# Kernel optimization log

Hardware: AMD Instinct MI355X
Metric: run time of the kernel (lower is better)

## Reference

```python
import jax, jax.numpy as jnp
import numpy as np

N_NODES = 50000
N_EDGES = 800000
D_IN = 64
F1 = 64
F2 = 64
D_HID = 100


def setup_inputs() -> dict:
    key = jax.random.key(0)
    ks = jax.random.split(key, 12)
    x = jax.random.normal(ks[0], (N_NODES, D_IN), dtype=jnp.float32)
    edge_src = jax.random.randint(ks[1], (N_EDGES,), 0, N_NODES, dtype=jnp.int32)
    edge_dst = jax.random.randint(ks[2], (N_EDGES,), 0, N_NODES, dtype=jnp.int32)
    # stands in for pre-normalized GCN adjacency values (D^-1/2 (A+I) D^-1/2)
    edge_weight = jax.random.uniform(ks[3], (N_EDGES,), dtype=jnp.float32)
    def glorot(k, shape):
        lim = np.sqrt(6.0 / (shape[0] + shape[1]))
        return jax.random.uniform(k, shape, jnp.float32, -lim, lim)
    W1 = glorot(ks[4], (D_IN, F1))
    b1 = jnp.zeros((F1,), jnp.float32)
    W2 = glorot(ks[5], (F1, F2))
    b2 = jnp.zeros((F2,), jnp.float32)
    Wd = glorot(ks[6], (F2, D_HID))
    bd = jnp.zeros((D_HID,), jnp.float32)
    Wo = glorot(ks[7], (D_HID, 1))
    bo = jnp.zeros((1,), jnp.float32)
    return {"x": x, "edge_src": edge_src, "edge_dst": edge_dst,
            "edge_weight": edge_weight, "W1": W1, "b1": b1, "W2": W2,
            "b2": b2, "Wd": Wd, "bd": bd, "Wo": Wo, "bo": bo}


def _gcn_conv(x, edge_src, edge_dst, edge_weight, W, b):
    # spektral GCNConv: out = swish(A_norm @ (X @ W) + b)
    h = x @ W                                        # [N, F]
    msg = h[edge_src] * edge_weight[:, None]          # [E, F] gather + scale
    agg = jax.ops.segment_sum(msg, edge_dst, num_segments=N_NODES)  # [N, F]
    return jax.nn.swish(agg + b)


def reference(x, edge_src, edge_dst, edge_weight, W1, b1, W2, b2, Wd, bd, Wo, bo):
    h = _gcn_conv(x, edge_src, edge_dst, edge_weight, W1, b1)
    h = _gcn_conv(h, edge_src, edge_dst, edge_weight, W2, b2)
    h = jax.nn.swish(h @ Wd + bd)                    # Dense(100, swish)
    return jax.nn.sigmoid(h @ Wo + bo)               # Dense(1, sigmoid) -> [N, 1]
```

## Files before the change

kernel.cpp:

```cpp
#include <hip/hip_runtime.h>
#include <hip/hip_fp16.h>

#define N_NODES 50000
#define N_EDGES 800000
#define D 64
#define DHID 100
#define NTILES (N_NODES / 16)
#define NCT 7
#define CAP 64
#define NGROUPS 4
#define NSLICES 780
#define FILL_BLOCKS (NGROUPS * NSLICES)
#define MM_BLOCKS ((NTILES + 3) / 4)
#define DST_PER_GROUP (N_NODES / NGROUPS)

typedef unsigned short ushort;
typedef unsigned int uint;
typedef __attribute__((ext_vector_type(8))) short s16x8;
typedef __attribute__((ext_vector_type(4))) float f32x4;

#define MFMA16(A, B, C) __builtin_amdgcn_mfma_f32_16x16x32_bf16((A), (B), (C), 0, 0, 0)

__device__ __forceinline__ float swishf(float x) { return x / (1.0f + __expf(-x)); }

__device__ __forceinline__ ushort f2bf(float f) {
    uint u = __float_as_uint(f);
    uint r = (u + 0x7fffu + ((u >> 16) & 1u)) >> 16;
    return (ushort)r;
}
__device__ __forceinline__ float bf2f(ushort h) { return __uint_as_float((uint)h << 16); }
__device__ __forceinline__ float bf_lo(uint d) { return __uint_as_float(d << 16); }
__device__ __forceinline__ float bf_hi(uint d) { return __uint_as_float(d & 0xffff0000u); }

__device__ __forceinline__ float hwf(uint e) {
    return __half2float(__ushort_as_half((ushort)(e >> 16)));
}

__device__ __forceinline__ void accum8(float* acc, uint4 v, float w) {
    acc[0] = fmaf(w, bf_lo(v.x), acc[0]);
    acc[1] = fmaf(w, bf_hi(v.x), acc[1]);
    acc[2] = fmaf(w, bf_lo(v.y), acc[2]);
    acc[3] = fmaf(w, bf_hi(v.y), acc[3]);
    acc[4] = fmaf(w, bf_lo(v.z), acc[4]);
    acc[5] = fmaf(w, bf_hi(v.z), acc[5]);
    acc[6] = fmaf(w, bf_lo(v.w), acc[6]);
    acc[7] = fmaf(w, bf_hi(v.w), acc[7]);
}

__device__ __forceinline__ void gather_node2(const ushort* __restrict__ H,
                                             const uint* __restrict__ bucket,
                                             int degv, int j, int fg, float* acc) {
#pragma unroll
    for (int t = 0; t < 8; ++t) acc[t] = 0.f;
    for (int base = 0; base < degv; base += 16) {
        int s0 = base + j * 4;
        if (s0 < degv) {
            uint4 e = *((const uint4*)(bucket + s0));
            float w0 = hwf(e.x);
            float w1 = (s0 + 1 < degv) ? hwf(e.y) : 0.f;
            float w2 = (s0 + 2 < degv) ? hwf(e.z) : 0.f;
            float w3 = (s0 + 3 < degv) ? hwf(e.w) : 0.f;
            uint s0i = min(e.x & 0xffffu, (uint)(N_NODES - 1));
            uint s1i = min(e.y & 0xffffu, (uint)(N_NODES - 1));
            uint s2i = min(e.z & 0xffffu, (uint)(N_NODES - 1));
            uint s3i = min(e.w & 0xffffu, (uint)(N_NODES - 1));
            uint4 v0 = *((const uint4*)(H + ((size_t)s0i << 6) + (fg << 3)));
            uint4 v1 = *((const uint4*)(H + ((size_t)s1i << 6) + (fg << 3)));
            uint4 v2 = *((const uint4*)(H + ((size_t)s2i << 6) + (fg << 3)));
            uint4 v3 = *((const uint4*)(H + ((size_t)s3i << 6) + (fg << 3)));
            accum8(acc, v0, w0);
            accum8(acc, v1, w1);
            accum8(acc, v2, w2);
            accum8(acc, v3, w3);
        }
    }
#pragma unroll
    for (int t = 0; t < 8; ++t) {
        acc[t] += __shfl_xor(acc[t], 8, 64);
        acc[t] += __shfl_xor(acc[t], 16, 64);
    }
}

__global__ __launch_bounds__(256) void fill_and_l1(const int* __restrict__ src,
                                                   const int* __restrict__ dst,
                                                   const float* __restrict__ w,
                                                   int* __restrict__ deg,
                                                   uint* __restrict__ csr,
                                                   const float* __restrict__ X,
                                                   const float* __restrict__ W,
                                                   const float* __restrict__ W2,
                                                   const float* __restrict__ Wd,
                                                   short* __restrict__ W2T2,
                                                   short* __restrict__ WdT2,
                                                   ushort* __restrict__ H) {
    __shared__ __align__(16) short sBT[2][D][72];
    int tid = threadIdx.x;

    if (blockIdx.x < FILL_BLOCKS) {
        const int g = blockIdx.x & (NGROUPS - 1);
        const int s = blockIdx.x >> 2;
        const int lo = g * DST_PER_GROUP;
        const int hi = lo + DST_PER_GROUP;
        for (int e = s * 256 + tid; e < N_EDGES; e += NSLICES * 256) {
            int d = __builtin_nontemporal_load(dst + e);
            if (d >= lo && d < hi) {
                float wval = __builtin_nontemporal_load(w + e);
                int sval = __builtin_nontemporal_load(src + e);
                uint hw = (uint)__half_as_ushort(__float2half_rn(wval));
                uint payload = (uint)sval | (hw << 16);
                int r = atomicAdd(&deg[d], 1);
                r = min(r, CAP - 1);
                csr[(d << 6) + r] = payload;
            }
        }
        return;
    }

    if (blockIdx.x >= FILL_BLOCKS + MM_BLOCKS) {
        if (blockIdx.x == FILL_BLOCKS + MM_BLOCKS) {
            for (int idx = tid; idx < D * D; idx += 256) {
                int k = idx >> 6, c = idx & 63;
                float wv = W2[idx];
                ushort hi = f2bf(wv);
                W2T2[(size_t)c * D + k] = (short)hi;
                W2T2[(size_t)(D + c) * D + k] = (short)f2bf(wv - bf2f(hi));
            }
        } else {
            for (int idx = tid; idx < NCT * 16 * D; idx += 256) {
                int jj = idx >> 6, k = idx & 63;
                float wv = (jj < DHID) ? Wd[k * DHID + jj] : 0.f;
                ushort hi = f2bf(wv);
                WdT2[(size_t)jj * D + k] = (short)hi;
                WdT2[(size_t)(NCT * 16 + jj) * D + k] = (short)f2bf(wv - bf2f(hi));
            }
        }
        return;
    }

    for (int idx = tid; idx < D * D; idx += 256) {
        int k = idx >> 6, c = idx & 63;
        float wv = W[idx];
        ushort hi = f2bf(wv);
        sBT[0][c][k] = (short)hi;
        sBT[1][c][k] = (short)f2bf(wv - bf2f(hi));
    }
    __syncthreads();
    int wv_ = tid >> 6, lane = tid & 63, quad = lane >> 4, m = lane & 15;
    int tile = min((blockIdx.x - FILL_BLOCKS) * 4 + wv_, NTILES - 1);
    int node0 = tile * 16;

    f32x4 acc[4] = {{0,0,0,0},{0,0,0,0},{0,0,0,0},{0,0,0,0}};
#pragma unroll
    for (int kt = 0; kt < 2; ++kt) {
        int k0 = kt * 32 + quad * 8;
        const float* xp = X + ((size_t)(node0 + m) << 6) + k0;
        f32x4 xa = __builtin_nontemporal_load((const f32x4*)xp);
        f32x4 xb = __builtin_nontemporal_load((const f32x4*)(xp + 4));
        float xv[8] = {xa[0], xa[1], xa[2], xa[3], xb[0], xb[1], xb[2], xb[3]};
        s16x8 ahi, alo;
#pragma unroll
        for (int jj = 0; jj < 8; ++jj) {
            ushort hi = f2bf(xv[jj]);
            ahi[jj] = (short)hi;
            alo[jj] = (short)f2bf(xv[jj] - bf2f(hi));
        }
#pragma unroll
        for (int ct = 0; ct < 4; ++ct) {
            int n = ct * 16 + m;
            s16x8 bhi = *((const s16x8*)&sBT[0][n][k0]);
            s16x8 blo = *((const s16x8*)&sBT[1][n][k0]);
            acc[ct] = MFMA16(ahi, bhi, acc[ct]);
            acc[ct] = MFMA16(ahi, blo, acc[ct]);
            acc[ct] = MFMA16(alo, bhi, acc[ct]);
        }
    }
    __syncthreads();
    short (*rep)[16][72] = (short(*)[16][72])&sBT[0][0][0];
#pragma unroll
    for (int ct = 0; ct < 4; ++ct)
#pragma unroll
        for (int r = 0; r < 4; ++r)
            rep[wv_][quad * 4 + r][ct * 16 + m] = (short)f2bf(acc[ct][r]);
#pragma unroll
    for (int half = 0; half < 2; ++half) {
        int r = (lane >> 3) + half * 8;
        int c0 = (lane & 7) * 8;
        s16x8 v = *((const s16x8*)&rep[wv_][r][c0]);
        *((s16x8*)(H + ((size_t)(node0 + r) << 6) + c0)) = v;
    }
}

__global__ __launch_bounds__(256) void gather_act(const ushort* __restrict__ H,
                                                  const int* __restrict__ deg,
                                                  const uint* __restrict__ csr,
                                                  const float* __restrict__ bias,
                                                  ushort* __restrict__ actOut) {
    int tid = threadIdx.x;
    int wave = tid >> 6, lane = tid & 63;
    int h = lane >> 5, j = (lane >> 3) & 3, fg = lane & 7;
    int node = blockIdx.x * 8 + wave * 2 + h;
    int degv = min(deg[node], CAP);
    const uint* bucket = csr + ((size_t)node << 6);

    float acc[8];
    gather_node2(H, bucket, degv, j, fg, acc);
    if (j == 0) {
        float4 ba = ((const float4*)bias)[fg * 2];
        float4 bb = ((const float4*)bias)[fg * 2 + 1];
        float r0 = swishf(acc[0] + ba.x);
        float r1 = swishf(acc[1] + ba.y);
        float r2 = swishf(acc[2] + ba.z);
        float r3 = swishf(acc[3] + ba.w);
        float r4 = swishf(acc[4] + bb.x);
        float r5 = swishf(acc[5] + bb.y);
        float r6 = swishf(acc[6] + bb.z);
        float r7 = swishf(acc[7] + bb.w);
        uint4 u;
        u.x = (uint)f2bf(r0) | ((uint)f2bf(r1) << 16);
        u.y = (uint)f2bf(r2) | ((uint)f2bf(r3) << 16);
        u.z = (uint)f2bf(r4) | ((uint)f2bf(r5) << 16);
        u.w = (uint)f2bf(r6) | ((uint)f2bf(r7) << 16);
        *((uint4*)(actOut + ((size_t)node << 6) + (fg << 3))) = u;
    }
}

__global__ __launch_bounds__(256) void gather_tail(const ushort* __restrict__ act1,
                                                   const int* __restrict__ deg,
                                                   const uint* __restrict__ csr,
                                                   const short* __restrict__ W2T2,
                                                   const float* __restrict__ b2,
                                                   const short* __restrict__ WdT2,
                                                   const float* __restrict__ bd,
                                                   const float* __restrict__ Wo,
                                                   const float* __restrict__ bo,
                                                   float* __restrict__ out) {
    __shared__ __align__(16) float sAgg[16][72];
    __shared__ __align__(16) short sAct2[16][72];
    __shared__ float sPart[4][16];
    int tid = threadIdx.x;
    int wv = tid >> 6, lane = tid & 63;
    int h = lane >> 5, j = (lane >> 3) & 3, fg = lane & 7;
    int quad = lane >> 4, m = lane & 15;
    int node0 = blockIdx.x * 16;

    for (int t = 0; t < 2; ++t) {
        int nl = wv * 4 + t * 2 + h;
        int node = node0 + nl;
        int degv = min(deg[node], CAP);
        const uint* bucket = csr + ((size_t)node << 6);
        float acc[8];
        gather_node2(act1, bucket, degv, j, fg, acc);
        if (j == 0) {
            float4 u0 = {acc[0], acc[1], acc[2], acc[3]};
            float4 u1 = {acc[4], acc[5], acc[6], acc[7]};
            *((float4*)&sAgg[nl][fg * 8]) = u0;
            *((float4*)&sAgg[nl][fg * 8 + 4]) = u1;
        }
    }
    __syncthreads();

    {
        f32x4 acc = {0, 0, 0, 0};
        int n = wv * 16 + m;
#pragma unroll
        for (int kt = 0; kt < 2; ++kt) {
            int k0 = kt * 32 + quad * 8;
            float4 xa = *((const float4*)&sAgg[m][k0]);
            float4 xb = *((const float4*)&sAgg[m][k0 + 4]);
            float xv[8] = {xa.x, xa.y, xa.z, xa.w, xb.x, xb.y, xb.z, xb.w};
            s16x8 ahi, alo;
#pragma unroll
            for (int jj = 0; jj < 8; ++jj) {
                ushort hi = f2bf(xv[jj]);
                ahi[jj] = (short)hi;
                alo[jj] = (short)f2bf(xv[jj] - bf2f(hi));
            }
            s16x8 bhi = *((const s16x8*)(W2T2 + (size_t)n * D + k0));
            s16x8 blo = *((const s16x8*)(W2T2 + (size_t)(D + n) * D + k0));
            acc = MFMA16(ahi, bhi, acc);
            acc = MFMA16(ahi, blo, acc);
            acc = MFMA16(alo, bhi, acc);
        }
        float bv = b2[n];
#pragma unroll
        for (int r = 0; r < 4; ++r)
            sAct2[quad * 4 + r][n] = (short)f2bf(swishf(acc[r] + bv));
    }
    __syncthreads();

    float part[4] = {0, 0, 0, 0};
#pragma unroll
    for (int cc = 0; cc < 2; ++cc) {
        int ct = wv + cc * 4;
        if (ct < NCT) {
            f32x4 acc = {0, 0, 0, 0};
            int n = ct * 16 + m;
#pragma unroll
            for (int kt = 0; kt < 2; ++kt) {
                int k0 = kt * 32 + quad * 8;
                s16x8 a = *((const s16x8*)&sAct2[m][k0]);
                s16x8 bhi = *((const s16x8*)(WdT2 + (size_t)n * D + k0));
                s16x8 blo = *((const s16x8*)(WdT2 + (size_t)(NCT * 16 + n) * D + k0));
                acc = MFMA16(a, bhi, acc);
                acc = MFMA16(a, blo, acc);
            }
            float bdv = (n < DHID) ? bd[n] : 0.f;
            float wov = (n < DHID) ? Wo[n] : 0.f;
#pragma unroll
            for (int r = 0; r < 4; ++r)
                part[r] = fmaf(swishf(acc[r] + bdv), wov, part[r]);
        }
    }
#pragma unroll
    for (int r = 0; r < 4; ++r) {
        part[r] += __shfl_xor(part[r], 1, 64);
        part[r] += __shfl_xor(part[r], 2, 64);
        part[r] += __shfl_xor(part[r], 4, 64);
        part[r] += __shfl_xor(part[r], 8, 64);
    }
    if (m == 0) {
#pragma unroll
        for (int r = 0; r < 4; ++r)
            sPart[wv][quad * 4 + r] = part[r];
    }
    __syncthreads();
    if (tid < 16) {
        float z = sPart[0][tid] + sPart[1][tid] + sPart[2][tid] + sPart[3][tid] + bo[0];
        out[node0 + tid] = 1.f / (1.f + __expf(-z));
    }
}

extern "C" void kernel_launch(void* const* d_in, const int* in_sizes, int n_in,
                              void* d_out, int out_size, void* d_ws, size_t ws_size,
                              hipStream_t stream) {
    const float* x   = (const float*)d_in[0];
    const int* esrc  = (const int*)d_in[1];
    const int* edst  = (const int*)d_in[2];
    const float* ew  = (const float*)d_in[3];
    const float* W1  = (const float*)d_in[4];
    const float* b1  = (const float*)d_in[5];
    const float* W2  = (const float*)d_in[6];
    const float* b2  = (const float*)d_in[7];
    const float* Wd  = (const float*)d_in[8];
    const float* bd  = (const float*)d_in[9];
    const float* Wo  = (const float*)d_in[10];
    const float* bo  = (const float*)d_in[11];
    float* out = (float*)d_out;

    char* ws = (char*)d_ws;
    ushort* H1   = (ushort*)ws;  ws += (size_t)N_NODES * D * sizeof(ushort);
    ushort* act1 = (ushort*)ws;  ws += (size_t)N_NODES * D * sizeof(ushort);
    uint* csr    = (uint*)ws;    ws += (size_t)N_NODES * CAP * sizeof(uint);
    int* deg     = (int*)ws;     ws += (size_t)N_NODES * sizeof(int);
    short* W2T2  = (short*)ws;   ws += (size_t)2 * D * D * sizeof(short);
    short* WdT2  = (short*)ws;   ws += (size_t)2 * NCT * 16 * D * sizeof(short);

    const int gBlocks = N_NODES / 8;

    hipMemsetAsync(deg, 0, (size_t)N_NODES * sizeof(int), stream);

    fill_and_l1<<<FILL_BLOCKS + MM_BLOCKS + 2, 256, 0, stream>>>(
        esrc, edst, ew, deg, csr, x, W1, W2, Wd, W2T2, WdT2, H1);

    gather_act<<<gBlocks, 256, 0, stream>>>(H1, deg, csr, b1, act1);

    gather_tail<<<NTILES, 256, 0, stream>>>(act1, deg, csr, W2T2, b2, WdT2, bd, Wo, bo, out);
}
```

Measured before the change: 181.0 us.

## Batch fill loads, prefetch first two gather chunks, widen tail block

The CSR fill loop becomes a fully unrolled batch of up to nine edges per thread, with twice as many destination groups. All dst loads are issued first, then the weight and src loads, then the atomics, so memory latency overlaps. The gather helper now loads the first 32 bucket entries and their feature rows before deg is known to be needed, and before any accumulation. This raises memory-level parallelism at the cost of more registers and some speculative loads. gather_tail moves to 512 threads, so each wave handles one node pair and one dense column tile, with no loops.

```diff
diff --git a/kernel.cpp b/kernel.cpp
--- a/kernel.cpp
+++ b/kernel.cpp
@@ -8,11 +8,13 @@
 #define NTILES (N_NODES / 16)
 #define NCT 7
 #define CAP 64
-#define NGROUPS 4
-#define NSLICES 780
+#define NGROUPS 8
+#define NSLICES 390
 #define FILL_BLOCKS (NGROUPS * NSLICES)
 #define MM_BLOCKS ((NTILES + 3) / 4)
 #define DST_PER_GROUP (N_NODES / NGROUPS)
+#define FSTRIDE (NSLICES * 256)
+#define KMAX 9
 
 typedef unsigned short ushort;
 typedef unsigned int uint;
@@ -49,10 +51,60 @@
 
 __device__ __forceinline__ void gather_node2(const ushort* __restrict__ H,
                                              const uint* __restrict__ bucket,
-                                             int degv, int j, int fg, float* acc) {
+                                             const int* __restrict__ degp,
+                                             int j, int fg, float* acc) {
 #pragma unroll
     for (int t = 0; t < 8; ++t) acc[t] = 0.f;
-    for (int base = 0; base < degv; base += 16) {
+    const int sA = j * 4, sB = 16 + j * 4;
+    uint4 eA = *((const uint4*)(bucket + sA));
+    uint4 eB = *((const uint4*)(bucket + sB));
+    int degv = min(*degp, CAP);
+
+    bool pA = sA < degv, pB = sB < degv;
+    uint4 vA0, vA1, vA2, vA3, vB0, vB1, vB2, vB3;
+    float wA0 = 0, wA1 = 0, wA2 = 0, wA3 = 0;
+    float wB0 = 0, wB1 = 0, wB2 = 0, wB3 = 0;
+    if (pA) {
+        wA0 = hwf(eA.x);
+        wA1 = (sA + 1 < degv) ? hwf(eA.y) : 0.f;
+        wA2 = (sA + 2 < degv) ? hwf(eA.z) : 0.f;
+        wA3 = (sA + 3 < degv) ? hwf(eA.w) : 0.f;
+        uint i0 = min(eA.x & 0xffffu, (uint)(N_NODES - 1));
+        uint i1 = min(eA.y & 0xffffu, (uint)(N_NODES - 1));
+        uint i2 = min(eA.z & 0xffffu, (uint)(N_NODES - 1));
+        uint i3 = min(eA.w & 0xffffu, (uint)(N_NODES - 1));
+        vA0 = *((const uint4*)(H + ((size_t)i0 << 6) + (fg << 3)));
+        vA1 = *((const uint4*)(H + ((size_t)i1 << 6) + (fg << 3)));
+        vA2 = *((const uint4*)(H + ((size_t)i2 << 6) + (fg << 3)));
+        vA3 = *((const uint4*)(H + ((size_t)i3 << 6) + (fg << 3)));
+    }
+    if (pB) {
+        wB0 = hwf(eB.x);
+        wB1 = (sB + 1 < degv) ? hwf(eB.y) : 0.f;
+        wB2 = (sB + 2 < degv) ? hwf(eB.z) : 0.f;
+        wB3 = (sB + 3 < degv) ? hwf(eB.w) : 0.f;
+        uint i0 = min(eB.x & 0xffffu, (uint)(N_NODES - 1));
+        uint i1 = min(eB.y & 0xffffu, (uint)(N_NODES - 1));
+        uint i2 = min(eB.z & 0xffffu, (uint)(N_NODES - 1));
+        uint i3 = min(eB.w & 0xffffu, (uint)(N_NODES - 1));
+        vB0 = *((const uint4*)(H + ((size_t)i0 << 6) + (fg << 3)));
+        vB1 = *((const uint4*)(H + ((size_t)i1 << 6) + (fg << 3)));
+        vB2 = *((const uint4*)(H + ((size_t)i2 << 6) + (fg << 3)));
+        vB3 = *((const uint4*)(H + ((size_t)i3 << 6) + (fg << 3)));
+    }
+    if (pA) {
+        accum8(acc, vA0, wA0);
+        accum8(acc, vA1, wA1);
+        accum8(acc, vA2, wA2);
+        accum8(acc, vA3, wA3);
+    }
+    if (pB) {
+        accum8(acc, vB0, wB0);
+        accum8(acc, vB1, wB1);
+        accum8(acc, vB2, wB2);
+        accum8(acc, vB3, wB3);
+    }
+    for (int base = 32; base < degv; base += 16) {
         int s0 = base + j * 4;
         if (s0 < degv) {
             uint4 e = *((const uint4*)(bucket + s0));
@@ -98,21 +150,39 @@
 
     if (blockIdx.x < FILL_BLOCKS) {
         const int g = blockIdx.x & (NGROUPS - 1);
-        const int s = blockIdx.x >> 2;
+        const int s = blockIdx.x >> 3;
         const int lo = g * DST_PER_GROUP;
-        const int hi = lo + DST_PER_GROUP;
-        for (int e = s * 256 + tid; e < N_EDGES; e += NSLICES * 256) {
-            int d = __builtin_nontemporal_load(dst + e);
-            if (d >= lo && d < hi) {
-                float wval = __builtin_nontemporal_load(w + e);
-                int sval = __builtin_nontemporal_load(src + e);
-                uint hw = (uint)__half_as_ushort(__float2half_rn(wval));
-                uint payload = (uint)sval | (hw << 16);
-                int r = atomicAdd(&deg[d], 1);
-                r = min(r, CAP - 1);
-                csr[(d << 6) + r] = payload;
+        const int e0 = s * 256 + tid;
+        int d[KMAX];
+        bool mk[KMAX];
+#pragma unroll
+        for (int k = 0; k < KMAX; ++k) {
+            int e = e0 + k * FSTRIDE;
+            int dv = (e < N_EDGES) ? __builtin_nontemporal_load(dst + e) : -1;
+            d[k] = dv;
+            mk[k] = ((uint)(dv - lo) < (uint)DST_PER_GROUP);
+        }
+        float wv9[KMAX];
+        int sv9[KMAX];
+#pragma unroll
+        for (int k = 0; k < KMAX; ++k)
+            if (mk[k]) {
+                int e = e0 + k * FSTRIDE;
+                wv9[k] = __builtin_nontemporal_load(w + e);
+                sv9[k] = __builtin_nontemporal_load(src + e);
             }
-        }
+        int r9[KMAX];
+#pragma unroll
+        for (int k = 0; k < KMAX; ++k)
+            if (mk[k]) r9[k] = atomicAdd(&deg[d[k]], 1);
+#pragma unroll
+        for (int k = 0; k < KMAX; ++k)
+            if (mk[k]) {
+                uint hw = (uint)__half_as_ushort(__float2half_rn(wv9[k]));
+                uint payload = (uint)sv9[k] | (hw << 16);
+                int r = min(r9[k], CAP - 1);
+                csr[(d[k] << 6) + r] = payload;
+            }
         return;
     }
 
@@ -199,11 +269,10 @@
     int wave = tid >> 6, lane = tid & 63;
     int h = lane >> 5, j = (lane >> 3) & 3, fg = lane & 7;
     int node = blockIdx.x * 8 + wave * 2 + h;
-    int degv = min(deg[node], CAP);
     const uint* bucket = csr + ((size_t)node << 6);
 
     float acc[8];
-    gather_node2(H, bucket, degv, j, fg, acc);
+    gather_node2(H, bucket, deg + node, j, fg, acc);
     if (j == 0) {
         float4 ba = ((const float4*)bias)[fg * 2];
         float4 bb = ((const float4*)bias)[fg * 2 + 1];
@@ -224,7 +293,7 @@
     }
 }
 
-__global__ __launch_bounds__(256) void gather_tail(const ushort* __restrict__ act1,
+__global__ __launch_bounds__(512) void gather_tail(const ushort* __restrict__ act1,
                                                    const int* __restrict__ deg,
                                                    const uint* __restrict__ csr,
                                                    const short* __restrict__ W2T2,
@@ -236,20 +305,19 @@
                                                    float* __restrict__ out) {
     __shared__ __align__(16) float sAgg[16][72];
     __shared__ __align__(16) short sAct2[16][72];
-    __shared__ float sPart[4][16];
+    __shared__ float sPart[8][16];
     int tid = threadIdx.x;
     int wv = tid >> 6, lane = tid & 63;
     int h = lane >> 5, j = (lane >> 3) & 3, fg = lane & 7;
     int quad = lane >> 4, m = lane & 15;
     int node0 = blockIdx.x * 16;
 
-    for (int t = 0; t < 2; ++t) {
-        int nl = wv * 4 + t * 2 + h;
+    {
+        int nl = wv * 2 + h;
         int node = node0 + nl;
-        int degv = min(deg[node], CAP);
         const uint* bucket = csr + ((size_t)node << 6);
         float acc[8];
-        gather_node2(act1, bucket, degv, j, fg, acc);
+        gather_node2(act1, bucket, deg + node, j, fg, acc);
         if (j == 0) {
             float4 u0 = {acc[0], acc[1], acc[2], acc[3]};
             float4 u1 = {acc[4], acc[5], acc[6], acc[7]};
@@ -259,7 +327,7 @@
     }
     __syncthreads();
 
-    {
+    if (wv < 4) {
         f32x4 acc = {0, 0, 0, 0};
         int n = wv * 16 + m;
 #pragma unroll
@@ -289,27 +357,23 @@
     __syncthreads();
 
     float part[4] = {0, 0, 0, 0};
-#pragma unroll
-    for (int cc = 0; cc < 2; ++cc) {
-        int ct = wv + cc * 4;
-        if (ct < NCT) {
-            f32x4 acc = {0, 0, 0, 0};
-            int n = ct * 16 + m;
-#pragma unroll
-            for (int kt = 0; kt < 2; ++kt) {
-                int k0 = kt * 32 + quad * 8;
-                s16x8 a = *((const s16x8*)&sAct2[m][k0]);
-                s16x8 bhi = *((const s16x8*)(WdT2 + (size_t)n * D + k0));
-                s16x8 blo = *((const s16x8*)(WdT2 + (size_t)(NCT * 16 + n) * D + k0));
-                acc = MFMA16(a, bhi, acc);
-                acc = MFMA16(a, blo, acc);
-            }
-            float bdv = (n < DHID) ? bd[n] : 0.f;
-            float wov = (n < DHID) ? Wo[n] : 0.f;
-#pragma unroll
-            for (int r = 0; r < 4; ++r)
-                part[r] = fmaf(swishf(acc[r] + bdv), wov, part[r]);
-        }
+    if (wv < NCT) {
+        f32x4 acc = {0, 0, 0, 0};
+        int n = wv * 16 + m;
+#pragma unroll
+        for (int kt = 0; kt < 2; ++kt) {
+            int k0 = kt * 32 + quad * 8;
+            s16x8 a = *((const s16x8*)&sAct2[m][k0]);
+            s16x8 bhi = *((const s16x8*)(WdT2 + (size_t)n * D + k0));
+            s16x8 blo = *((const s16x8*)(WdT2 + (size_t)(NCT * 16 + n) * D + k0));
+            acc = MFMA16(a, bhi, acc);
+            acc = MFMA16(a, blo, acc);
+        }
+        float bdv = (n < DHID) ? bd[n] : 0.f;
+        float wov = (n < DHID) ? Wo[n] : 0.f;
+#pragma unroll
+        for (int r = 0; r < 4; ++r)
+            part[r] = fmaf(swishf(acc[r] + bdv), wov, part[r]);
     }
 #pragma unroll
     for (int r = 0; r < 4; ++r) {
@@ -325,7 +389,9 @@
     }
     __syncthreads();
     if (tid < 16) {
-        float z = sPart[0][tid] + sPart[1][tid] + sPart[2][tid] + sPart[3][tid] + bo[0];
+        float z = bo[0];
+#pragma unroll
+        for (int i = 0; i < 8; ++i) z += sPart[i][tid];
         out[node0 + tid] = 1.f / (1.f + __expf(-z));
     }
 }
@@ -364,5 +430,5 @@
 
     gather_act<<<gBlocks, 256, 0, stream>>>(H1, deg, csr, b1, act1);
 
-    gather_tail<<<NTILES, 256, 0, stream>>>(act1, deg, csr, W2T2, b2, WdT2, bd, Wo, bo, out);
-}
+    gather_tail<<<NTILES, 512, 0, stream>>>(act1, deg, csr, W2T2, b2, WdT2, bd, Wo, bo, out);
+}
```

Result: slower. 195.4 us (+7.9%).
